# Performance work log

Measured on AMD Instinct MI355X. Metric: run time of the kernel, lower is better.

The kernel has to match this reference:

```python
import jax, jax.numpy as jnp
import numpy as np

B, T, C, H = 2, 2048, 1024, 16
D = C // H  # head_dim = 64


def setup_inputs() -> dict:
    key = jax.random.key(0)
    ks = jax.random.split(key, 5)
    x = jax.random.normal(ks[0], (B, T, C), dtype=jnp.float32)
    # fused QKV projection: Linear(C, 3C)
    W_qkv = jax.random.normal(ks[1], (C, 3 * C), dtype=jnp.float32) / np.sqrt(C)
    b_qkv = jax.random.normal(ks[2], (3 * C,), dtype=jnp.float32) * 0.02
    # output projection: Linear(C, C)
    W_proj = jax.random.normal(ks[3], (C, C), dtype=jnp.float32) / np.sqrt(C)
    b_proj = jax.random.normal(ks[4], (C,), dtype=jnp.float32) * 0.02
    return {"x": x, "W_qkv": W_qkv, "b_qkv": b_qkv, "W_proj": W_proj, "b_proj": b_proj}


def reference(x, W_qkv, b_qkv, W_proj, b_proj):
    # fused QKV projection
    qkv = jnp.einsum("btc,cd->btd", x, W_qkv) + b_qkv  # [B,T,3C]
    q, k, v = jnp.split(qkv, 3, axis=-1)
    # [B,T,C] -> [B,H,T,D]
    def to_heads(t):
        return t.reshape(B, T, H, D).transpose(0, 2, 1, 3)
    q, k, v = to_heads(q), to_heads(k), to_heads(v)
    # causal scaled dot-product attention (SDPA default scale = 1/sqrt(head_dim))
    scale = 1.0 / np.sqrt(D).astype(np.float32)
    scores = jnp.einsum("bhqd,bhkd->bhqk", q, k) * scale  # [B,H,T,T]
    causal = jnp.tril(jnp.ones((T, T), dtype=bool))
    scores = jnp.where(causal, scores, jnp.finfo(scores.dtype).min)
    attn = jax.nn.softmax(scores, axis=-1)
    out = jnp.einsum("bhqk,bhkd->bhqd", attn, v)  # [B,H,T,D]
    out = out.transpose(0, 2, 1, 3).reshape(B, T, C)
    # output projection
    return jnp.einsum("btc,cd->btd", out, W_proj) + b_proj
```

## Files before the change

kernel.cpp:

```cpp
#include <hip/hip_runtime.h>
#include <hip/hip_bf16.h>

typedef __attribute__((ext_vector_type(8))) __bf16 bf16x8;
typedef __attribute__((ext_vector_type(8))) short short8;
typedef __attribute__((ext_vector_type(4))) float f32x4;
typedef __attribute__((ext_vector_type(4))) short sh4;

typedef __attribute__((address_space(1))) void GVoid;
typedef __attribute__((address_space(3))) void LVoid;

#define NEGBIG (-1e30f)
#define SCL 0.18033688011112042f

constexpr int TT = 2048, CC = 1024, HH = 16, DD = 64, C3 = 3072;

__device__ __forceinline__ unsigned short f2bf(float f) {
  unsigned int i = __float_as_uint(f);
  return (unsigned short)((i + 0x7FFFu + ((i >> 16) & 1u)) >> 16);
}
__device__ __forceinline__ unsigned short f2bf_tr(float f) {
  return (unsigned short)(__float_as_uint(f) >> 16);
}
__device__ __forceinline__ void async16(const void* g, void* l) {
  __builtin_amdgcn_global_load_lds((GVoid*)g, (LVoid*)l, 16, 0, 0);
}

__global__ __launch_bounds__(256) void cvt_bf16(
    const float* __restrict__ in, unsigned short* __restrict__ out, int n8)
{
  const int i = blockIdx.x * 256 + threadIdx.x;
  if (i >= n8) return;
  const float* p = in + (size_t)i * 8;
  f32x4 a = *(const f32x4*)p, b = *(const f32x4*)(p + 4);
  sh4 r0, r1;
  ((unsigned short*)&r0)[0] = f2bf(a[0]); ((unsigned short*)&r0)[1] = f2bf(a[1]);
  ((unsigned short*)&r0)[2] = f2bf(a[2]); ((unsigned short*)&r0)[3] = f2bf(a[3]);
  ((unsigned short*)&r1)[0] = f2bf(b[0]); ((unsigned short*)&r1)[1] = f2bf(b[1]);
  ((unsigned short*)&r1)[2] = f2bf(b[2]); ((unsigned short*)&r1)[3] = f2bf(b[3]);
  *(sh4*)(out + (size_t)i * 8) = r0;
  *(sh4*)(out + (size_t)i * 8 + 4) = r1;
}

__global__ __launch_bounds__(256) void transpose_cvt(
    const float* __restrict__ in, unsigned short* __restrict__ out, int R, int Cd)
{
  __shared__ __align__(16) unsigned short tile[64 * 72];
  const int r0 = blockIdx.y * 64, c0 = blockIdx.x * 64;
  const int tid = threadIdx.x;
#pragma unroll
  for (int r = 0; r < 2; ++r) {
    const int elem = r * 2048 + tid * 8;
    const int ii = elem >> 6, jj = elem & 63;
    const float* p = in + (size_t)(r0 + ii) * Cd + c0 + jj;
    f32x4 a = *(const f32x4*)p, b = *(const f32x4*)(p + 4);
    short8 v;
    ((unsigned short*)&v)[0] = f2bf(a[0]); ((unsigned short*)&v)[1] = f2bf(a[1]);
    ((unsigned short*)&v)[2] = f2bf(a[2]); ((unsigned short*)&v)[3] = f2bf(a[3]);
    ((unsigned short*)&v)[4] = f2bf(b[0]); ((unsigned short*)&v)[5] = f2bf(b[1]);
    ((unsigned short*)&v)[6] = f2bf(b[2]); ((unsigned short*)&v)[7] = f2bf(b[3]);
    *(short8*)&tile[ii * 72 + jj] = v;
  }
  __syncthreads();
#pragma unroll
  for (int r = 0; r < 2; ++r) {
    const int elem = r * 2048 + tid * 8;
    const int jj = elem >> 6, ii0 = elem & 63;
    short8 v;
#pragma unroll
    for (int e = 0; e < 8; ++e) ((unsigned short*)&v)[e] = tile[(ii0 + e) * 72 + jj];
    *(short8*)&out[(size_t)(c0 + jj) * R + r0 + ii0] = v;
  }
}

template <int MODE>
__global__ __launch_bounds__(256) void gemm_bt(
    const unsigned short* __restrict__ A,
    const unsigned short* __restrict__ Bt,
    const float* __restrict__ bias,
    void* __restrict__ Cp, unsigned short* __restrict__ Vt,
    int M, int N, int K, int lda)
{
  __shared__ __align__(16) unsigned short sA[128 * 32];
  __shared__ __align__(16) unsigned short sB[128 * 32];
  const int tid = threadIdx.x;
  const int w = tid >> 6, l = tid & 63, ln = l & 15, quad = l >> 4;
  const int wm = w >> 1, wn = w & 1;
  const int m0 = blockIdx.y * 128, n0 = blockIdx.x * 128;
  f32x4 acc[4][4] = {};

  for (int k0 = 0; k0 < K; k0 += 32) {
    __syncthreads();
#pragma unroll
    for (int r = 0; r < 2; ++r) {
      const int elem = r * 2048 + tid * 8;
      const int ar = elem >> 5, ac = elem & 31;
      async16(A  + (size_t)(m0 + ar) * lda + k0 + ac, sA + r * 2048 + w * 512);
      async16(Bt + (size_t)(n0 + ar) * K   + k0 + ac, sB + r * 2048 + w * 512);
    }
    __syncthreads();

    bf16x8 af[4], bfr[4];
#pragma unroll
    for (int i = 0; i < 4; i++)
      af[i] = *(const bf16x8*)&sA[(wm * 64 + i * 16 + ln) * 32 + quad * 8];
#pragma unroll
    for (int j = 0; j < 4; j++)
      bfr[j] = *(const bf16x8*)&sB[(wn * 64 + j * 16 + ln) * 32 + quad * 8];
#pragma unroll
    for (int i = 0; i < 4; i++)
#pragma unroll
      for (int j = 0; j < 4; j++)
        acc[i][j] = __builtin_amdgcn_mfma_f32_16x16x32_bf16(af[i], bfr[j], acc[i][j], 0, 0, 0);
  }

  float bj[4];
#pragma unroll
  for (int j = 0; j < 4; j++) bj[j] = bias[n0 + wn * 64 + j * 16 + ln];

#pragma unroll
  for (int i = 0; i < 4; i++)
#pragma unroll
    for (int g = 0; g < 4; ++g) {
      const int gm = m0 + wm * 64 + i * 16 + quad * 4 + g;
#pragma unroll
      for (int j = 0; j < 4; j++) {
        const int gn = n0 + wn * 64 + j * 16 + ln;
        float v = acc[i][j][g] + bj[j];
        if (MODE == 0) {
          if (gn < 2048) {
            if (gn < 1024) v *= SCL;
            ((unsigned short*)Cp)[(size_t)gm * 2048 + gn] = f2bf(v);
          } else {
            const int hh = (gn >> 6) & 15, dd = gn & 63;
            const int bb = gm >> 11, t = gm & 2047;
            Vt[((size_t)((bb * HH + hh) * DD + dd)) * TT + t] = f2bf(v);
          }
        } else {
          ((float*)Cp)[(size_t)gm * N + gn] = v;
        }
      }
    }
}

__global__ __launch_bounds__(512) void attn128(
    unsigned short* __restrict__ QK, const unsigned short* __restrict__ Vt)
{
  __shared__ __align__(16) unsigned short kt[2][64 * 72];
  __shared__ __align__(16) unsigned short vt[2][80 * 72];
  __shared__ __align__(16) unsigned short pt[8][16 * 72];
  const int pair = blockIdx.x, bh = blockIdx.y;
  const int b = bh >> 4, h = bh & 15;
  const int tid = threadIdx.x, w = tid >> 6, l = tid & 63, ln = l & 15, quad = l >> 4;
  unsigned short*       Qp = QK + (size_t)b * TT * 2048 + h * DD;
  const unsigned short* Kp = QK + (size_t)b * TT * 2048 + CC + h * DD;
  const unsigned short* Vh = Vt + (size_t)bh * DD * TT;
  const int si = tid >> 3, so = (tid & 7) * 8;

  for (int idx = tid; idx < 16 * 72; idx += 512) {
    const unsigned short v = (idx < 72) ? (unsigned short)0x3F80 : (unsigned short)0;
    vt[0][64 * 72 + idx] = v;
    vt[1][64 * 72 + idx] = v;
  }

  for (int ph = 0; ph < 2; ++ph) {
    const int qt = ph ? 15 - pair : pair;
    const int qrow = qt * 128 + w * 16 + ln;
    bf16x8 qf0 = *(const bf16x8*)&Qp[(size_t)qrow * 2048 + quad * 8];
    bf16x8 qf1 = *(const bf16x8*)&Qp[(size_t)qrow * 2048 + 32 + quad * 8];

    f32x4 oacc[4] = {};
    f32x4 lacc = {};
    const int qg = qt * 128 + w * 16 + quad * 4;
    const int wfirst = qt * 128 + w * 16, wlast = wfirst + 15;
    const int kbmax = 2 * qt + 1;

    *(short8*)&kt[0][si * 72 + so] = *(const short8*)&Kp[(size_t)si * 2048 + so];
    *(short8*)&vt[0][si * 72 + so] = *(const short8*)&Vh[(size_t)si * TT + so];
    __syncthreads();

    for (int kb = 0; kb <= kbmax; ++kb) {
      const int cur = kb & 1;
      short8 pk, pv;
      if (kb < kbmax) {
        pk = *(const short8*)&Kp[(size_t)((kb + 1) * 64 + si) * 2048 + so];
        pv = *(const short8*)&Vh[(size_t)si * TT + (kb + 1) * 64 + so];
      }
      if (kb * 64 <= wlast) {
        f32x4 sacc[4] = {};
#pragma unroll
        for (int n = 0; n < 4; n++) {
          bf16x8 bk0 = *(const bf16x8*)&kt[cur][(n * 16 + ln) * 72 + quad * 8];
          bf16x8 bk1 = *(const bf16x8*)&kt[cur][(n * 16 + ln) * 72 + 32 + quad * 8];
          sacc[n] = __builtin_amdgcn_mfma_f32_16x16x32_bf16(qf0, bk0, sacc[n], 0, 0, 0);
          sacc[n] = __builtin_amdgcn_mfma_f32_16x16x32_bf16(qf1, bk1, sacc[n], 0, 0, 0);
        }
        if (kb * 64 + 63 > wfirst) {
#pragma unroll
          for (int n = 0; n < 4; n++) {
            const int keyg = kb * 64 + n * 16 + ln;
#pragma unroll
            for (int g = 0; g < 4; ++g)
              if (keyg > qg + g) sacc[n][g] = NEGBIG;
          }
        }
#pragma unroll
        for (int n = 0; n < 4; n++)
#pragma unroll
          for (int g = 0; g < 4; ++g)
            pt[w][(quad * 4 + g) * 72 + n * 16 + ln] = f2bf_tr(exp2f(sacc[n][g]));
        __builtin_amdgcn_wave_barrier();
        bf16x8 pf0 = *(const bf16x8*)&pt[w][ln * 72 + quad * 8];
        bf16x8 pf1 = *(const bf16x8*)&pt[w][ln * 72 + 32 + quad * 8];
#pragma unroll
        for (int n = 0; n < 4; n++) {
          bf16x8 bv0 = *(const bf16x8*)&vt[cur][(n * 16 + ln) * 72 + quad * 8];
          bf16x8 bv1 = *(const bf16x8*)&vt[cur][(n * 16 + ln) * 72 + 32 + quad * 8];
          oacc[n] = __builtin_amdgcn_mfma_f32_16x16x32_bf16(pf0, bv0, oacc[n], 0, 0, 0);
          oacc[n] = __builtin_amdgcn_mfma_f32_16x16x32_bf16(pf1, bv1, oacc[n], 0, 0, 0);
        }
        bf16x8 bl0 = *(const bf16x8*)&vt[cur][(64 + ln) * 72 + quad * 8];
        bf16x8 bl1 = *(const bf16x8*)&vt[cur][(64 + ln) * 72 + 32 + quad * 8];
        lacc = __builtin_amdgcn_mfma_f32_16x16x32_bf16(pf0, bl0, lacc, 0, 0, 0);
        lacc = __builtin_amdgcn_mfma_f32_16x16x32_bf16(pf1, bl1, lacc, 0, 0, 0);
      }
      if (kb < kbmax) {
        *(short8*)&kt[1 - cur][si * 72 + so] = pk;
        *(short8*)&vt[1 - cur][si * 72 + so] = pv;
      }
      __syncthreads();
    }
#pragma unroll
    for (int g = 0; g < 4; ++g) {
      const float lv = __shfl(lacc[g], l & 48);
      const float inv = 1.0f / lv;
      const int t = qg + g;
#pragma unroll
      for (int n = 0; n < 4; n++)
        Qp[(size_t)t * 2048 + n * 16 + ln] = f2bf(oacc[n][g] * inv);
    }
  }
}

extern "C" void kernel_launch(void* const* d_in, const int* in_sizes, int n_in,
                              void* d_out, int out_size, void* d_ws, size_t ws_size,
                              hipStream_t stream)
{
  (void)in_sizes; (void)n_in; (void)out_size; (void)ws_size;
  const float* x     = (const float*)d_in[0];
  const float* Wqkv  = (const float*)d_in[1];
  const float* bqkv  = (const float*)d_in[2];
  const float* Wproj = (const float*)d_in[3];
  const float* bproj = (const float*)d_in[4];

  unsigned short* QK     = (unsigned short*)d_ws;
  unsigned short* WqkvT  = QK + (size_t)4096 * 2048;
  unsigned short* WprojT = WqkvT;
  unsigned short* Vt = (unsigned short*)d_out;
  unsigned short* xb = Vt + (size_t)32 * 64 * 2048;

  cvt_bf16<<<dim3(4096 * 1024 / 8 / 256), 256, 0, stream>>>(x, xb, 4096 * 1024 / 8);
  transpose_cvt<<<dim3(C3 / 64, CC / 64), 256, 0, stream>>>(Wqkv, WqkvT, CC, C3);
  gemm_bt<0><<<dim3(C3 / 128, 4096 / 128), 256, 0, stream>>>(
      xb, WqkvT, bqkv, QK, Vt, 4096, C3, CC, CC);
  transpose_cvt<<<dim3(CC / 64, CC / 64), 256, 0, stream>>>(Wproj, WprojT, CC, CC);
  attn128<<<dim3(8, 2 * HH), 512, 0, stream>>>(QK, Vt);
  gemm_bt<1><<<dim3(CC / 128, 4096 / 128), 256, 0, stream>>>(
      QK, WprojT, bproj, d_out, nullptr, 4096, CC, CC, 2048);
}
```

Before: 208.1 us.

## Restructure attention to 4 waves of 32 query rows, one tile per block

Each attention block now handles a single 128-row query tile with 4 waves of 32 rows each, instead of 8 waves of 16 rows processing a pair of tiles. Every K/V fragment read from LDS feeds two MFMAs, halving LDS traffic per MFMA. The grid doubles to 16x32 blocks, ordered heaviest-first, which replaces the paired-tile load balancing. The row-sum ones vector now lives in a register instead of extra LDS rows. The cost is more registers per wave and fewer waves per block to hide latency.

Result: slower. 233.9 us (+12.4%).

```diff
diff --git a/kernel.cpp b/kernel.cpp
--- a/kernel.cpp
+++ b/kernel.cpp
@@ -142,13 +142,13 @@
     }
 }
 
-__global__ __launch_bounds__(512) void attn128(
+__global__ __launch_bounds__(256) void attn128(
     unsigned short* __restrict__ QK, const unsigned short* __restrict__ Vt)
 {
   __shared__ __align__(16) unsigned short kt[2][64 * 72];
-  __shared__ __align__(16) unsigned short vt[2][80 * 72];
-  __shared__ __align__(16) unsigned short pt[8][16 * 72];
-  const int pair = blockIdx.x, bh = blockIdx.y;
+  __shared__ __align__(16) unsigned short vt[2][64 * 72];
+  __shared__ __align__(16) unsigned short pt[4][32 * 72];
+  const int qt = 15 - blockIdx.x, bh = blockIdx.y;
   const int b = bh >> 4, h = bh & 15;
   const int tid = threadIdx.x, w = tid >> 6, l = tid & 63, ln = l & 15, quad = l >> 4;
   unsigned short*       Qp = QK + (size_t)b * TT * 2048 + h * DD;
@@ -156,89 +156,114 @@
   const unsigned short* Vh = Vt + (size_t)bh * DD * TT;
   const int si = tid >> 3, so = (tid & 7) * 8;
 
-  for (int idx = tid; idx < 16 * 72; idx += 512) {
-    const unsigned short v = (idx < 72) ? (unsigned short)0x3F80 : (unsigned short)0;
-    vt[0][64 * 72 + idx] = v;
-    vt[1][64 * 72 + idx] = v;
-  }
-
-  for (int ph = 0; ph < 2; ++ph) {
-    const int qt = ph ? 15 - pair : pair;
-    const int qrow = qt * 128 + w * 16 + ln;
-    bf16x8 qf0 = *(const bf16x8*)&Qp[(size_t)qrow * 2048 + quad * 8];
-    bf16x8 qf1 = *(const bf16x8*)&Qp[(size_t)qrow * 2048 + 32 + quad * 8];
-
-    f32x4 oacc[4] = {};
-    f32x4 lacc = {};
-    const int qg = qt * 128 + w * 16 + quad * 4;
-    const int wfirst = qt * 128 + w * 16, wlast = wfirst + 15;
-    const int kbmax = 2 * qt + 1;
-
-    *(short8*)&kt[0][si * 72 + so] = *(const short8*)&Kp[(size_t)si * 2048 + so];
-    *(short8*)&vt[0][si * 72 + so] = *(const short8*)&Vh[(size_t)si * TT + so];
-    __syncthreads();
-
-    for (int kb = 0; kb <= kbmax; ++kb) {
-      const int cur = kb & 1;
-      short8 pk, pv;
-      if (kb < kbmax) {
-        pk = *(const short8*)&Kp[(size_t)((kb + 1) * 64 + si) * 2048 + so];
-        pv = *(const short8*)&Vh[(size_t)si * TT + (kb + 1) * 64 + so];
-      }
-      if (kb * 64 <= wlast) {
-        f32x4 sacc[4] = {};
-#pragma unroll
-        for (int n = 0; n < 4; n++) {
-          bf16x8 bk0 = *(const bf16x8*)&kt[cur][(n * 16 + ln) * 72 + quad * 8];
-          bf16x8 bk1 = *(const bf16x8*)&kt[cur][(n * 16 + ln) * 72 + 32 + quad * 8];
-          sacc[n] = __builtin_amdgcn_mfma_f32_16x16x32_bf16(qf0, bk0, sacc[n], 0, 0, 0);
-          sacc[n] = __builtin_amdgcn_mfma_f32_16x16x32_bf16(qf1, bk1, sacc[n], 0, 0, 0);
-        }
-        if (kb * 64 + 63 > wfirst) {
+  bf16x8 blf;
+#pragma unroll
+  for (int e = 0; e < 8; ++e)
+    ((unsigned short*)&blf)[e] = (ln == 0) ? (unsigned short)0x3F80 : (unsigned short)0;
+
+  const int wfirst = qt * 128 + w * 32;
+  bf16x8 qf[2][2];
+#pragma unroll
+  for (int i = 0; i < 2; ++i) {
+    const int qrow = wfirst + i * 16 + ln;
+    qf[i][0] = *(const bf16x8*)&Qp[(size_t)qrow * 2048 + quad * 8];
+    qf[i][1] = *(const bf16x8*)&Qp[(size_t)qrow * 2048 + 32 + quad * 8];
+  }
+
+  f32x4 oacc[4][2] = {};
+  f32x4 lacc[2] = {};
+  const int wlast = wfirst + 31;
+  const int kbmax = 2 * qt + 1;
+
+  *(short8*)&kt[0][si * 72 + so]        = *(const short8*)&Kp[(size_t)si * 2048 + so];
+  *(short8*)&kt[0][(si + 32) * 72 + so] = *(const short8*)&Kp[(size_t)(si + 32) * 2048 + so];
+  *(short8*)&vt[0][si * 72 + so]        = *(const short8*)&Vh[(size_t)si * TT + so];
+  *(short8*)&vt[0][(si + 32) * 72 + so] = *(const short8*)&Vh[(size_t)(si + 32) * TT + so];
+  __syncthreads();
+
+  for (int kb = 0; kb <= kbmax; ++kb) {
+    const int cur = kb & 1;
+    short8 pk0, pk1, pv0, pv1;
+    if (kb < kbmax) {
+      pk0 = *(const short8*)&Kp[(size_t)((kb + 1) * 64 + si) * 2048 + so];
+      pk1 = *(const short8*)&Kp[(size_t)((kb + 1) * 64 + si + 32) * 2048 + so];
+      pv0 = *(const short8*)&Vh[(size_t)si * TT + (kb + 1) * 64 + so];
+      pv1 = *(const short8*)&Vh[(size_t)(si + 32) * TT + (kb + 1) * 64 + so];
+    }
+    if (kb * 64 <= wlast) {
+      f32x4 sacc[2][4] = {};
+#pragma unroll
+      for (int n = 0; n < 4; n++) {
+        bf16x8 bk0 = *(const bf16x8*)&kt[cur][(n * 16 + ln) * 72 + quad * 8];
+        bf16x8 bk1 = *(const bf16x8*)&kt[cur][(n * 16 + ln) * 72 + 32 + quad * 8];
+#pragma unroll
+        for (int i = 0; i < 2; ++i) {
+          sacc[i][n] = __builtin_amdgcn_mfma_f32_16x16x32_bf16(qf[i][0], bk0, sacc[i][n], 0, 0, 0);
+          sacc[i][n] = __builtin_amdgcn_mfma_f32_16x16x32_bf16(qf[i][1], bk1, sacc[i][n], 0, 0, 0);
+        }
+      }
+      if (kb * 64 + 63 > wfirst) {
+#pragma unroll
+        for (int i = 0; i < 2; ++i) {
+          const int qgi = wfirst + i * 16 + quad * 4;
 #pragma unroll
           for (int n = 0; n < 4; n++) {
             const int keyg = kb * 64 + n * 16 + ln;
 #pragma unroll
             for (int g = 0; g < 4; ++g)
-              if (keyg > qg + g) sacc[n][g] = NEGBIG;
+              if (keyg > qgi + g) sacc[i][n][g] = NEGBIG;
           }
         }
+      }
+#pragma unroll
+      for (int i = 0; i < 2; ++i)
 #pragma unroll
         for (int n = 0; n < 4; n++)
 #pragma unroll
           for (int g = 0; g < 4; ++g)
-            pt[w][(quad * 4 + g) * 72 + n * 16 + ln] = f2bf_tr(exp2f(sacc[n][g]));
-        __builtin_amdgcn_wave_barrier();
-        bf16x8 pf0 = *(const bf16x8*)&pt[w][ln * 72 + quad * 8];
-        bf16x8 pf1 = *(const bf16x8*)&pt[w][ln * 72 + 32 + quad * 8];
-#pragma unroll
-        for (int n = 0; n < 4; n++) {
-          bf16x8 bv0 = *(const bf16x8*)&vt[cur][(n * 16 + ln) * 72 + quad * 8];
-          bf16x8 bv1 = *(const bf16x8*)&vt[cur][(n * 16 + ln) * 72 + 32 + quad * 8];
-          oacc[n] = __builtin_amdgcn_mfma_f32_16x16x32_bf16(pf0, bv0, oacc[n], 0, 0, 0);
-          oacc[n] = __builtin_amdgcn_mfma_f32_16x16x32_bf16(pf1, bv1, oacc[n], 0, 0, 0);
-        }
-        bf16x8 bl0 = *(const bf16x8*)&vt[cur][(64 + ln) * 72 + quad * 8];
-        bf16x8 bl1 = *(const bf16x8*)&vt[cur][(64 + ln) * 72 + 32 + quad * 8];
-        lacc = __builtin_amdgcn_mfma_f32_16x16x32_bf16(pf0, bl0, lacc, 0, 0, 0);
-        lacc = __builtin_amdgcn_mfma_f32_16x16x32_bf16(pf1, bl1, lacc, 0, 0, 0);
-      }
-      if (kb < kbmax) {
-        *(short8*)&kt[1 - cur][si * 72 + so] = pk;
-        *(short8*)&vt[1 - cur][si * 72 + so] = pv;
-      }
-      __syncthreads();
-    }
+            pt[w][(i * 16 + quad * 4 + g) * 72 + n * 16 + ln] = f2bf_tr(exp2f(sacc[i][n][g]));
+      __builtin_amdgcn_wave_barrier();
+      bf16x8 pf[2][2];
+#pragma unroll
+      for (int i = 0; i < 2; ++i) {
+        pf[i][0] = *(const bf16x8*)&pt[w][(i * 16 + ln) * 72 + quad * 8];
+        pf[i][1] = *(const bf16x8*)&pt[w][(i * 16 + ln) * 72 + 32 + quad * 8];
+      }
+#pragma unroll
+      for (int n = 0; n < 4; n++) {
+        bf16x8 bv0 = *(const bf16x8*)&vt[cur][(n * 16 + ln) * 72 + quad * 8];
+        bf16x8 bv1 = *(const bf16x8*)&vt[cur][(n * 16 + ln) * 72 + 32 + quad * 8];
+#pragma unroll
+        for (int i = 0; i < 2; ++i) {
+          oacc[n][i] = __builtin_amdgcn_mfma_f32_16x16x32_bf16(pf[i][0], bv0, oacc[n][i], 0, 0, 0);
+          oacc[n][i] = __builtin_amdgcn_mfma_f32_16x16x32_bf16(pf[i][1], bv1, oacc[n][i], 0, 0, 0);
+        }
+      }
+#pragma unroll
+      for (int i = 0; i < 2; ++i) {
+        lacc[i] = __builtin_amdgcn_mfma_f32_16x16x32_bf16(pf[i][0], blf, lacc[i], 0, 0, 0);
+        lacc[i] = __builtin_amdgcn_mfma_f32_16x16x32_bf16(pf[i][1], blf, lacc[i], 0, 0, 0);
+      }
+    }
+    if (kb < kbmax) {
+      *(short8*)&kt[1 - cur][si * 72 + so]        = pk0;
+      *(short8*)&kt[1 - cur][(si + 32) * 72 + so] = pk1;
+      *(short8*)&vt[1 - cur][si * 72 + so]        = pv0;
+      *(short8*)&vt[1 - cur][(si + 32) * 72 + so] = pv1;
+    }
+    __syncthreads();
+  }
+#pragma unroll
+  for (int i = 0; i < 2; ++i)
 #pragma unroll
     for (int g = 0; g < 4; ++g) {
-      const float lv = __shfl(lacc[g], l & 48);
+      const float lv = __shfl(lacc[i][g], l & 48);
       const float inv = 1.0f / lv;
-      const int t = qg + g;
+      const int t = wfirst + i * 16 + quad * 4 + g;
 #pragma unroll
       for (int n = 0; n < 4; n++)
-        Qp[(size_t)t * 2048 + n * 16 + ln] = f2bf(oacc[n][g] * inv);
-    }
-  }
+        Qp[(size_t)t * 2048 + n * 16 + ln] = f2bf(oacc[n][i][g] * inv);
+    }
 }
 
 extern "C" void kernel_launch(void* const* d_in, const int* in_sizes, int n_in,
@@ -263,7 +288,7 @@
   gemm_bt<0><<<dim3(C3 / 128, 4096 / 128), 256, 0, stream>>>(
       xb, WqkvT, bqkv, QK, Vt, 4096, C3, CC, CC);
   transpose_cvt<<<dim3(CC / 64, CC / 64), 256, 0, stream>>>(Wproj, WprojT, CC, CC);
-  attn128<<<dim3(8, 2 * HH), 512, 0, stream>>>(QK, Vt);
+  attn128<<<dim3(16, 2 * HH), 256, 0, stream>>>(QK, Vt);
   gemm_bt<1><<<dim3(CC / 128, 4096 / 128), 256, 0, stream>>>(
       QK, WprojT, bproj, d_out, nullptr, 4096, CC, CC, 2048);
 }
```
